# Optimization experiments

Measured on AMD Instinct MI355X. Metric: run time of the kernel, lower is better.

## Reference

```python
import jax, jax.numpy as jnp
import numpy as np

WINDOW = (2, 7, 7)
NUM_HEADS = 4
DIM = 128


def _relative_position_index(ws):
    d, h, w = ws
    coords = np.stack(np.meshgrid(np.arange(d), np.arange(h), np.arange(w), indexing='ij'))  # (3,d,h,w)
    cf = coords.reshape(3, -1)  # (3, N)
    rel = cf[:, :, None] - cf[:, None, :]  # (3, N, N)
    rel = rel.transpose(1, 2, 0).astype(np.int64)
    rel[:, :, 0] += d - 1
    rel[:, :, 1] += h - 1
    rel[:, :, 2] += w - 1
    rel[:, :, 0] *= (2 * h - 1) * (2 * w - 1)
    rel[:, :, 1] *= 2 * w - 1
    return rel.sum(-1).astype(np.int32)  # (N, N)


def setup_inputs() -> dict:
    key = jax.random.key(0)
    ks = jax.random.split(key, 6)
    N = WINDOW[0] * WINDOW[1] * WINDOW[2]  # 98
    B_, nW, C = 4096, 64, DIM
    x = jax.random.normal(ks[0], (B_, N, C), dtype=jnp.float32)
    mask = jax.random.normal(ks[1], (nW, N, N), dtype=jnp.float32)
    qkv_w = jax.random.normal(ks[2], (3 * C, C), dtype=jnp.float32) * (C ** -0.5)
    proj_w = jax.random.normal(ks[3], (C, C), dtype=jnp.float32) * (C ** -0.5)
    proj_b = jax.random.normal(ks[4], (C,), dtype=jnp.float32) * 0.02
    n_bias = (2 * WINDOW[0] - 1) * (2 * WINDOW[1] - 1) * (2 * WINDOW[2] - 1)  # 507
    bias_table = jax.random.normal(ks[5], (n_bias, NUM_HEADS), dtype=jnp.float32) * 0.02
    rel_index = jnp.asarray(_relative_position_index(WINDOW))
    return {"x": x, "mask": mask, "qkv_w": qkv_w, "proj_w": proj_w,
            "proj_b": proj_b, "bias_table": bias_table, "rel_index": rel_index}


def reference(x, mask, qkv_w, proj_w, proj_b, bias_table, rel_index):
    B_, N, C = x.shape
    H = NUM_HEADS
    hd = C // H
    scale = hd ** -0.5
    # qkv projection (no bias), split heads -> (3, B_, H, N, hd)
    qkv = (x @ qkv_w.T).reshape(B_, N, 3, H, hd).transpose(2, 0, 3, 1, 4)
    q, k, v = qkv[0] * scale, qkv[1], qkv[2]
    attn = jnp.einsum('bhnd,bhmd->bhnm', q, k)  # (B_, H, N, N)
    # gathered relative position bias -> (H, N, N)
    bias = bias_table[rel_index.reshape(-1)].reshape(N, N, H).transpose(2, 0, 1)
    attn = attn + bias[None]
    nW = mask.shape[0]
    attn = attn.reshape(B_ // nW, nW, H, N, N) + mask[None, :, None]
    attn = jax.nn.softmax(attn.reshape(B_, H, N, N), axis=-1)
    out = jnp.einsum('bhnm,bhmd->bhnd', attn, v)  # (B_, H, N, hd)
    out = out.transpose(0, 2, 1, 3).reshape(B_, N, C)
    return out @ proj_w.T + proj_b
```

## Files before the change

### kernel.cpp

```cpp
#include <hip/hip_runtime.h>

typedef __attribute__((ext_vector_type(8))) short bf8;
typedef __attribute__((ext_vector_type(4))) float f4;
typedef __attribute__((ext_vector_type(16))) float f16v;
typedef __attribute__((ext_vector_type(2))) unsigned int u32x2;
typedef __attribute__((ext_vector_type(4))) unsigned int u32x4;

#define MFMA16(A,B,C) __builtin_amdgcn_mfma_f32_16x16x32_bf16(A,B,C,0,0,0)
#define MFMA32(A,B,C) __builtin_amdgcn_mfma_f32_32x32x16_bf16(A,B,C,0,0,0)

#define NTOK 98
#define SROW 136
#define SCALE 0.17677669529663687f

__device__ __forceinline__ unsigned short bfu(float f) {
  union { float f; unsigned u; } un; un.f = f;
  unsigned r = un.u + 0x7FFFu + ((un.u >> 16) & 1u);
  return (unsigned short)(r >> 16);
}
__device__ __forceinline__ unsigned cvtpk(float a, float b) {
  unsigned r;
  asm("v_cvt_pk_bf16_f32 %0, %1, %2" : "=v"(r) : "v"(a), "v"(b));
  return r;
}

__global__ void prep_kernel(const float* __restrict__ qkv_w,
                            const float* __restrict__ proj_w,
                            const float* __restrict__ bias_table,
                            const int* __restrict__ rel_index,
                            const float* __restrict__ mask,
                            unsigned short* __restrict__ wq,
                            unsigned short* __restrict__ wp,
                            float* __restrict__ bsmall,
                            float* __restrict__ bm, int use_bm) {
  const int T1 = 384*128, T2 = T1 + 128*128;
  const int TS = 4*128*112;
  const int T3 = T2 + TS;
  const int TB = 64*4*128*112;
  const int total = T3 + (use_bm ? TB : 0);
  for (int idx = blockIdx.x*blockDim.x + threadIdx.x; idx < total;
       idx += gridDim.x*blockDim.x) {
    if (idx < T1)      wq[idx] = bfu(qkv_w[idx]);
    else if (idx < T2) wp[idx - T1] = bfu(proj_w[idx - T1]);
    else if (idx < T3) {
      int t = idx - T2;
      int m = t % 112, n = (t/112) & 127, h = t / (112*128);
      float v;
      if (m >= NTOK)      v = -1e30f;
      else if (n >= NTOK) v = 0.f;
      else                v = bias_table[rel_index[n*98+m]*4 + h];
      bsmall[t] = v;
    } else {
      int t = idx - T3;
      int m = t % 112; int r = t / 112;
      int n = r & 127; r >>= 7;
      int h = r & 3;   int w = r >> 2;
      float v;
      if (m >= NTOK)      v = -1e30f;
      else if (n >= NTOK) v = 0.f;
      else v = bias_table[rel_index[n*98+m]*4 + h] + mask[(size_t)w*9604 + n*98 + m];
      bm[t] = v;
    }
  }
}

template<int USE_BM>
__launch_bounds__(1024, 1)
__global__ void wattn_kernel(const float* __restrict__ x,
                             const float* __restrict__ mask,
                             const float* __restrict__ proj_b,
                             const unsigned short* __restrict__ wqkv,
                             const unsigned short* __restrict__ wproj,
                             const float* __restrict__ bsmall,
                             const float* __restrict__ bm,
                             float* __restrict__ out) {
  __shared__ unsigned short xb[128*SROW];
  __shared__ unsigned short qb[128*SROW];
  __shared__ unsigned short kb[128*SROW];
  __shared__ unsigned short vt[128*SROW];

  const int b = blockIdx.x, tid = threadIdx.x;
  const int wid = tid >> 6, lane = tid & 63;
  const int g = lane >> 4, c = lane & 15;

  for (int i = tid; i < 14*SROW; i += 1024) xb[98*SROW + i] = 0;
  for (int i = tid; i < 16*SROW; i += 1024) { qb[112*SROW + i] = 0; kb[112*SROW + i] = 0; }

  const float* xp = x + (size_t)b * (NTOK*128);
  for (int i = tid; i < (NTOK*128)/4; i += 1024) {
    float4 v4 = ((const float4*)xp)[i];
    int e = i*4, n = e >> 7, cc = e & 127;
    u32x2 u; u[0] = cvtpk(v4.x, v4.y); u[1] = cvtpk(v4.z, v4.w);
    *(u32x2*)&xb[n*SROW + cc] = u;
  }
  __syncthreads();

  for (int k3 = 0; k3 < 3; ++k3) {
    const int u = wid + 16*k3;
    const int ot = u >> 1, half = u & 1;
    const int ib = half ? 4 : 0, ni = half ? 3 : 4;
    if (ot < 16) {
      const unsigned short* wptr = wqkv + (size_t)(ot*16 + c)*128;
      f4 acc[4] = {};
      #pragma unroll
      for (int kk = 0; kk < 4; ++kk) {
        bf8 wf = *(const bf8*)(wptr + kk*32 + g*8);
        #pragma unroll
        for (int i = 0; i < 4; ++i) if (i < ni) {
          bf8 xf = *(const bf8*)(&xb[((ib+i)*16 + c)*SROW + kk*32 + g*8]);
          acc[i] = MFMA16(wf, xf, acc[i]);
        }
      }
      unsigned short* dst = (ot < 8) ? qb : kb;
      const int col = (ot & 7)*16 + g*4;
      const float sc = (ot < 8) ? SCALE : 1.f;
      #pragma unroll
      for (int i = 0; i < 4; ++i) if (i < ni) {
        u32x2 uu;
        uu[0] = cvtpk(acc[i][0]*sc, acc[i][1]*sc);
        uu[1] = cvtpk(acc[i][2]*sc, acc[i][3]*sc);
        *(u32x2*)&dst[((ib+i)*16 + c)*SROW + col] = uu;
      }
    } else {
      const int ov = ot - 16;
      const unsigned short* wptr = wqkv + (size_t)(256 + ov*16 + c)*128;
      f4 acc[4] = {};
      #pragma unroll
      for (int kk = 0; kk < 4; ++kk) {
        bf8 wf = *(const bf8*)(wptr + kk*32 + g*8);
        #pragma unroll
        for (int i = 0; i < 4; ++i) if (i < ni) {
          bf8 xf = *(const bf8*)(&xb[((ib+i)*16 + c)*SROW + kk*32 + g*8]);
          acc[i] = MFMA16(xf, wf, acc[i]);
        }
      }
      #pragma unroll
      for (int i = 0; i < 4; ++i) if (i < ni) {
        u32x2 uu;
        uu[0] = cvtpk(acc[i][0], acc[i][1]);
        uu[1] = cvtpk(acc[i][2], acc[i][3]);
        *(u32x2*)&vt[(ov*16 + c)*SROW + (ib+i)*16 + g*4] = uu;
      }
    }
  }
  __syncthreads();

  {
    const int hh = wid & 3, i32 = wid >> 2;
    const int l31 = lane & 31, hl = lane >> 5;
    const int n = i32*32 + l31;

    f16v sj[4];
    const float* bmp = USE_BM ? (bm + ((size_t)((b & 63)*4 + hh)*128 + n)*112)
                              : (bsmall + ((size_t)hh*128 + n)*112);
    #pragma unroll
    for (int j = 0; j < 4; ++j)
      #pragma unroll
      for (int a = 0; a < 4; ++a) {
        f4 t;
        if (j == 3 && a >= 2) t = (f4){-1e30f, -1e30f, -1e30f, -1e30f};
        else t = *(const f4*)(bmp + j*32 + a*8 + hl*4);
        sj[j][4*a+0] = t[0]; sj[j][4*a+1] = t[1];
        sj[j][4*a+2] = t[2]; sj[j][4*a+3] = t[3];
      }
    if (!USE_BM && n < NTOK) {
      const float* mw = mask + (size_t)(b & 63)*9604 + n*98;
      #pragma unroll
      for (int j = 0; j < 4; ++j)
        #pragma unroll
        for (int a = 0; a < 4; ++a) {
          if (j == 3 && a >= 2) continue;
          #pragma unroll
          for (int bb = 0; bb < 4; ++bb) {
            int m = j*32 + a*8 + hl*4 + bb;
            if (m < NTOK) sj[j][4*a+bb] += mw[m];
          }
        }
    }
    #pragma unroll
    for (int kd = 0; kd < 2; ++kd) {
      bf8 qf = *(const bf8*)(&qb[n*SROW + hh*32 + kd*16 + hl*8]);
      #pragma unroll
      for (int j = 0; j < 4; ++j) {
        bf8 kf = *(const bf8*)(&kb[(j*32 + l31)*SROW + hh*32 + kd*16 + hl*8]);
        sj[j] = MFMA32(kf, qf, sj[j]);
      }
    }
    float sum = 0.f;
    #pragma unroll
    for (int j = 0; j < 4; ++j)
      #pragma unroll
      for (int r = 0; r < 16; ++r) { float e = __expf(sj[j][r]); sj[j][r] = e; sum += e; }
    sum += __shfl_xor(sum, 32);
    const float inv = 1.f / sum;
    unsigned P2[4][4][2];
    #pragma unroll
    for (int j = 0; j < 4; ++j)
      #pragma unroll
      for (int a = 0; a < 4; ++a) {
        P2[j][a][0] = cvtpk(sj[j][4*a+0], sj[j][4*a+1]);
        P2[j][a][1] = cvtpk(sj[j][4*a+2], sj[j][4*a+3]);
      }
    f16v acc = {0.f,0.f,0.f,0.f,0.f,0.f,0.f,0.f,0.f,0.f,0.f,0.f,0.f,0.f,0.f,0.f};
    #pragma unroll
    for (int km = 0; km < 7; ++km) {
      const int j = km >> 1, a0 = 2*(km & 1);
      bf8 vf = *(const bf8*)(&vt[(hh*32 + l31)*SROW + km*16 + hl*8]);
      unsigned o0 = P2[j][a0][0],   o1 = P2[j][a0][1];
      unsigned o2 = P2[j][a0+1][0], o3 = P2[j][a0+1][1];
      unsigned s0 = __shfl_xor(o0, 32), s1 = __shfl_xor(o1, 32);
      unsigned s2 = __shfl_xor(o2, 32), s3 = __shfl_xor(o3, 32);
      u32x4 pw;
      pw[0] = hl ? s2 : o0;  pw[1] = hl ? s3 : o1;
      pw[2] = hl ? o2 : s0;  pw[3] = hl ? o3 : s1;
      acc = MFMA32(vf, *(bf8*)&pw, acc);
    }
    #pragma unroll
    for (int a = 0; a < 4; ++a) {
      u32x2 uu;
      uu[0] = cvtpk(acc[4*a+0]*inv, acc[4*a+1]*inv);
      uu[1] = cvtpk(acc[4*a+2]*inv, acc[4*a+3]*inv);
      *(u32x2*)&xb[n*SROW + hh*32 + a*8 + hl*4] = uu;
    }
  }
  __syncthreads();

  for (int k3 = 0; k3 < 4; ++k3) {
    const int t = wid + 16*k3;
    if (t < 56) {
      const int i = t >> 3, ot = t & 7;
      const unsigned short* wptr = wproj + (size_t)(ot*16 + c)*128;
      f4 acc = {0.f, 0.f, 0.f, 0.f};
      #pragma unroll
      for (int kk = 0; kk < 4; ++kk) {
        bf8 wf = *(const bf8*)(wptr + kk*32 + g*8);
        bf8 xf = *(const bf8*)(&xb[(i*16 + c)*SROW + kk*32 + g*8]);
        acc = MFMA16(wf, xf, acc);
      }
      const int n2 = i*16 + c;
      if (n2 < NTOK) {
        f4 pb4 = *(const f4*)(proj_b + ot*16 + g*4);
        f4 o4 = {acc[0]+pb4[0], acc[1]+pb4[1], acc[2]+pb4[2], acc[3]+pb4[3]};
        *(f4*)(out + (size_t)b*(NTOK*128) + n2*128 + ot*16 + g*4) = o4;
      }
    }
  }
}

extern "C" void kernel_launch(void* const* d_in, const int* in_sizes, int n_in,
                              void* d_out, int out_size, void* d_ws, size_t ws_size,
                              hipStream_t stream) {
  const float* x          = (const float*)d_in[0];
  const float* mask       = (const float*)d_in[1];
  const float* qkv_w      = (const float*)d_in[2];
  const float* proj_w     = (const float*)d_in[3];
  const float* proj_b     = (const float*)d_in[4];
  const float* bias_table = (const float*)d_in[5];
  const int*   rel_index  = (const int*)d_in[6];

  unsigned short* wq = (unsigned short*)d_ws;
  unsigned short* wp = wq + 384*128;
  float* bsmall = (float*)((char*)d_ws + 131072);
  float* bm     = (float*)((char*)d_ws + 360448);

  const size_t need = 360448u + (size_t)64*4*128*112*4;
  const int use_bm = (ws_size >= need) ? 1 : 0;

  prep_kernel<<<2048, 256, 0, stream>>>(qkv_w, proj_w, bias_table, rel_index, mask,
                                        wq, wp, bsmall, bm, use_bm);
  if (use_bm)
    wattn_kernel<1><<<4096, 1024, 0, stream>>>(x, mask, proj_b, wq, wp, bsmall, bm,
                                               (float*)d_out);
  else
    wattn_kernel<0><<<4096, 1024, 0, stream>>>(x, mask, proj_b, wq, wp, bsmall, bm,
                                               (float*)d_out);
}
```

Baseline: 295.0 us.

## Store bias+mask in fp16, prefetch x and bias early, use exp2 softmax

```diff
diff --git a/kernel.cpp b/kernel.cpp
--- a/kernel.cpp
+++ b/kernel.cpp
@@ -11,7 +11,8 @@
 
 #define NTOK 98
 #define SROW 136
-#define SCALE 0.17677669529663687f
+#define LOG2E 1.4426950408889634f
+#define QSCALE (0.17677669529663687f * LOG2E)
 
 __device__ __forceinline__ unsigned short bfu(float f) {
   union { float f; unsigned u; } un; un.f = f;
@@ -22,6 +23,9 @@
   unsigned r;
   asm("v_cvt_pk_bf16_f32 %0, %1, %2" : "=v"(r) : "v"(a), "v"(b));
   return r;
+}
+__device__ __forceinline__ float h2f(unsigned short u) {
+  return (float)__builtin_bit_cast(_Float16, u);
 }
 
 __global__ void prep_kernel(const float* __restrict__ qkv_w,
@@ -32,7 +36,7 @@
                             unsigned short* __restrict__ wq,
                             unsigned short* __restrict__ wp,
                             float* __restrict__ bsmall,
-                            float* __restrict__ bm, int use_bm) {
+                            unsigned short* __restrict__ bmh, int use_bm) {
   const int T1 = 384*128, T2 = T1 + 128*128;
   const int TS = 4*128*112;
   const int T3 = T2 + TS;
@@ -48,7 +52,7 @@
       float v;
       if (m >= NTOK)      v = -1e30f;
       else if (n >= NTOK) v = 0.f;
-      else                v = bias_table[rel_index[n*98+m]*4 + h];
+      else                v = bias_table[rel_index[n*98+m]*4 + h] * LOG2E;
       bsmall[t] = v;
     } else {
       int t = idx - T3;
@@ -58,8 +62,8 @@
       float v;
       if (m >= NTOK)      v = -1e30f;
       else if (n >= NTOK) v = 0.f;
-      else v = bias_table[rel_index[n*98+m]*4 + h] + mask[(size_t)w*9604 + n*98 + m];
-      bm[t] = v;
+      else v = (bias_table[rel_index[n*98+m]*4 + h] + mask[(size_t)w*9604 + n*98 + m]) * LOG2E;
+      bmh[t] = __builtin_bit_cast(unsigned short, (_Float16)v);
     }
   }
 }
@@ -72,7 +76,7 @@
                              const unsigned short* __restrict__ wqkv,
                              const unsigned short* __restrict__ wproj,
                              const float* __restrict__ bsmall,
-                             const float* __restrict__ bm,
+                             const unsigned short* __restrict__ bmh,
                              float* __restrict__ out) {
   __shared__ unsigned short xb[128*SROW];
   __shared__ unsigned short qb[128*SROW];
@@ -82,16 +86,49 @@
   const int b = blockIdx.x, tid = threadIdx.x;
   const int wid = tid >> 6, lane = tid & 63;
   const int g = lane >> 4, c = lane & 15;
+  const int hh = wid & 3, i32 = wid >> 2;
+  const int l31 = lane & 31, hl = lane >> 5;
+  const int n = i32*32 + l31;
+
+  const float* xp = x + (size_t)b * (NTOK*128);
+  const float4* xp4 = (const float4*)xp;
+  float4 xv0 = xp4[tid];
+  float4 xv1 = xp4[tid + 1024];
+  float4 xv2 = xp4[tid + 2048];
+  float4 xv3;
+  const bool has3 = tid < 64;
+  if (has3) xv3 = xp4[tid + 3072];
+
+  ushort4 bmr[14];
+  if (USE_BM) {
+    const unsigned short* bp = bmh + ((size_t)((b & 63)*4 + hh)*128 + n)*112;
+    #pragma unroll
+    for (int j = 0; j < 3; ++j)
+      #pragma unroll
+      for (int a = 0; a < 4; ++a)
+        bmr[j*4+a] = *(const ushort4*)(bp + j*32 + a*8 + hl*4);
+    bmr[12] = *(const ushort4*)(bp + 96 + hl*4);
+    bmr[13] = *(const ushort4*)(bp + 96 + 8 + hl*4);
+  }
 
   for (int i = tid; i < 14*SROW; i += 1024) xb[98*SROW + i] = 0;
   for (int i = tid; i < 16*SROW; i += 1024) { qb[112*SROW + i] = 0; kb[112*SROW + i] = 0; }
 
-  const float* xp = x + (size_t)b * (NTOK*128);
-  for (int i = tid; i < (NTOK*128)/4; i += 1024) {
-    float4 v4 = ((const float4*)xp)[i];
-    int e = i*4, n = e >> 7, cc = e & 127;
-    u32x2 u; u[0] = cvtpk(v4.x, v4.y); u[1] = cvtpk(v4.z, v4.w);
-    *(u32x2*)&xb[n*SROW + cc] = u;
+  {
+    int e = tid*4, nn = e >> 7, cc = e & 127;
+    u32x2 u; u[0] = cvtpk(xv0.x, xv0.y); u[1] = cvtpk(xv0.z, xv0.w);
+    *(u32x2*)&xb[nn*SROW + cc] = u;
+    e = (tid+1024)*4; nn = e >> 7; cc = e & 127;
+    u[0] = cvtpk(xv1.x, xv1.y); u[1] = cvtpk(xv1.z, xv1.w);
+    *(u32x2*)&xb[nn*SROW + cc] = u;
+    e = (tid+2048)*4; nn = e >> 7; cc = e & 127;
+    u[0] = cvtpk(xv2.x, xv2.y); u[1] = cvtpk(xv2.z, xv2.w);
+    *(u32x2*)&xb[nn*SROW + cc] = u;
+    if (has3) {
+      e = (tid+3072)*4; nn = e >> 7; cc = e & 127;
+      u[0] = cvtpk(xv3.x, xv3.y); u[1] = cvtpk(xv3.z, xv3.w);
+      *(u32x2*)&xb[nn*SROW + cc] = u;
+    }
   }
   __syncthreads();
 
@@ -113,7 +150,7 @@
       }
       unsigned short* dst = (ot < 8) ? qb : kb;
       const int col = (ot & 7)*16 + g*4;
-      const float sc = (ot < 8) ? SCALE : 1.f;
+      const float sc = (ot < 8) ? QSCALE : 1.f;
       #pragma unroll
       for (int i = 0; i < 4; ++i) if (i < ni) {
         u32x2 uu;
@@ -146,22 +183,24 @@
   __syncthreads();
 
   {
-    const int hh = wid & 3, i32 = wid >> 2;
-    const int l31 = lane & 31, hl = lane >> 5;
-    const int n = i32*32 + l31;
-
     f16v sj[4];
-    const float* bmp = USE_BM ? (bm + ((size_t)((b & 63)*4 + hh)*128 + n)*112)
-                              : (bsmall + ((size_t)hh*128 + n)*112);
     #pragma unroll
     for (int j = 0; j < 4; ++j)
       #pragma unroll
       for (int a = 0; a < 4; ++a) {
-        f4 t;
-        if (j == 3 && a >= 2) t = (f4){-1e30f, -1e30f, -1e30f, -1e30f};
-        else t = *(const f4*)(bmp + j*32 + a*8 + hl*4);
-        sj[j][4*a+0] = t[0]; sj[j][4*a+1] = t[1];
-        sj[j][4*a+2] = t[2]; sj[j][4*a+3] = t[3];
+        if (j == 3 && a >= 2) {
+          sj[j][4*a+0] = -1e30f; sj[j][4*a+1] = -1e30f;
+          sj[j][4*a+2] = -1e30f; sj[j][4*a+3] = -1e30f;
+        } else if (USE_BM) {
+          ushort4 u = bmr[(j < 3) ? (j*4+a) : (12+a)];
+          sj[j][4*a+0] = h2f(u.x); sj[j][4*a+1] = h2f(u.y);
+          sj[j][4*a+2] = h2f(u.z); sj[j][4*a+3] = h2f(u.w);
+        } else {
+          const float* bmp = bsmall + ((size_t)hh*128 + n)*112;
+          f4 t = *(const f4*)(bmp + j*32 + a*8 + hl*4);
+          sj[j][4*a+0] = t[0]; sj[j][4*a+1] = t[1];
+          sj[j][4*a+2] = t[2]; sj[j][4*a+3] = t[3];
+        }
       }
     if (!USE_BM && n < NTOK) {
       const float* mw = mask + (size_t)(b & 63)*9604 + n*98;
@@ -173,10 +212,11 @@
           #pragma unroll
           for (int bb = 0; bb < 4; ++bb) {
             int m = j*32 + a*8 + hl*4 + bb;
-            if (m < NTOK) sj[j][4*a+bb] += mw[m];
+            if (m < NTOK) sj[j][4*a+bb] += mw[m] * LOG2E;
           }
         }
     }
+    __builtin_amdgcn_s_setprio(1);
     #pragma unroll
     for (int kd = 0; kd < 2; ++kd) {
       bf8 qf = *(const bf8*)(&qb[n*SROW + hh*32 + kd*16 + hl*8]);
@@ -186,11 +226,12 @@
         sj[j] = MFMA32(kf, qf, sj[j]);
       }
     }
+    __builtin_amdgcn_s_setprio(0);
     float sum = 0.f;
     #pragma unroll
     for (int j = 0; j < 4; ++j)
       #pragma unroll
-      for (int r = 0; r < 16; ++r) { float e = __expf(sj[j][r]); sj[j][r] = e; sum += e; }
+      for (int r = 0; r < 16; ++r) { float e = exp2f(sj[j][r]); sj[j][r] = e; sum += e; }
     sum += __shfl_xor(sum, 32);
     const float inv = 1.f / sum;
     unsigned P2[4][4][2];
@@ -202,6 +243,7 @@
         P2[j][a][1] = cvtpk(sj[j][4*a+2], sj[j][4*a+3]);
       }
     f16v acc = {0.f,0.f,0.f,0.f,0.f,0.f,0.f,0.f,0.f,0.f,0.f,0.f,0.f,0.f,0.f,0.f};
+    __builtin_amdgcn_s_setprio(1);
     #pragma unroll
     for (int km = 0; km < 7; ++km) {
       const int j = km >> 1, a0 = 2*(km & 1);
@@ -215,6 +257,7 @@
       pw[2] = hl ? o2 : s0;  pw[3] = hl ? o3 : s1;
       acc = MFMA32(vf, *(bf8*)&pw, acc);
     }
+    __builtin_amdgcn_s_setprio(0);
     #pragma unroll
     for (int a = 0; a < 4; ++a) {
       u32x2 uu;
@@ -261,17 +304,17 @@
   unsigned short* wq = (unsigned short*)d_ws;
   unsigned short* wp = wq + 384*128;
   float* bsmall = (float*)((char*)d_ws + 131072);
-  float* bm     = (float*)((char*)d_ws + 360448);
-
-  const size_t need = 360448u + (size_t)64*4*128*112*4;
+  unsigned short* bmh = (unsigned short*)((char*)d_ws + 360448);
+
+  const size_t need = 360448u + (size_t)64*4*128*112*2;
   const int use_bm = (ws_size >= need) ? 1 : 0;
 
   prep_kernel<<<2048, 256, 0, stream>>>(qkv_w, proj_w, bias_table, rel_index, mask,
-                                        wq, wp, bsmall, bm, use_bm);
+                                        wq, wp, bsmall, bmh, use_bm);
   if (use_bm)
-    wattn_kernel<1><<<4096, 1024, 0, stream>>>(x, mask, proj_b, wq, wp, bsmall, bm,
+    wattn_kernel<1><<<4096, 1024, 0, stream>>>(x, mask, proj_b, wq, wp, bsmall, bmh,
                                                (float*)d_out);
   else
-    wattn_kernel<0><<<4096, 1024, 0, stream>>>(x, mask, proj_b, wq, wp, bsmall, bm,
+    wattn_kernel<0><<<4096, 1024, 0, stream>>>(x, mask, proj_b, wq, wp, bsmall, bmh,
                                                (float*)d_out);
 }
```

After: 320.0 us. 1.08x slower.
